# Kernel optimization log

Measured on AMD Instinct MI355X. Metric: run time of the kernel, lower is better.

Reference implementation:

```python
import jax, jax.numpy as jnp
import numpy as np

DIM = 192
NUM_HEADS = 8
EPS = 1e-12  # F.normalize default eps


def setup_inputs() -> dict:
    key = jax.random.key(0)
    ks = jax.random.split(key, 6)
    b, c, h, w = 8, DIM, 128, 128
    scale = 1.0 / np.sqrt(DIM)  # conv2d default init scale (approx)
    return {
        "input": jax.random.normal(ks[0], (b, c, h, w), dtype=jnp.float32),
        "color": jax.random.normal(ks[1], (b, c, h, w), dtype=jnp.float32),
        "Wq": jax.random.normal(ks[2], (DIM, DIM), dtype=jnp.float32) * scale,
        "Wk": jax.random.normal(ks[3], (DIM, DIM), dtype=jnp.float32) * scale,
        "Wv": jax.random.normal(ks[4], (DIM, DIM), dtype=jnp.float32) * scale,
        "Wo": jax.random.normal(ks[5], (DIM, DIM), dtype=jnp.float32) * scale,
    }


def _proj(x, W):
    # 1x1 conv (bias=False) == channel GEMM: [b,c,h,w] x [out,c] -> [b,out,h,w]
    return jnp.einsum('bchw,oc->bohw', x, W)


def _l2norm(x):
    n = jnp.sqrt(jnp.sum(x * x, axis=-1, keepdims=True))
    return x / jnp.maximum(n, EPS)


def reference(input, color, Wq, Wk, Wv, Wo):
    b, c, h, w = input.shape
    head = NUM_HEADS
    dh = c // head
    hw = h * w
    # q from color, k/v from input
    q = _proj(color, Wq).reshape(b, head, dh, hw)
    k = _proj(input, Wk).reshape(b, head, dh, hw)
    v = _proj(input, Wv).reshape(b, head, dh, hw)
    q = _l2norm(q)
    k = _l2norm(k)
    # transposed (channel) attention: [b,head,dh,dh]
    attn = jnp.einsum('bhcn,bhdn->bhcd', q, k)
    attn = jax.nn.softmax(attn, axis=-1)
    out = jnp.einsum('bhcd,bhdn->bhcn', attn, v)  # [b,head,dh,hw]
    out = out.reshape(b, c, h, w)
    return _proj(out, Wo)
```

## Files before the change

kernel.cpp:

```cpp
#include <hip/hip_runtime.h>
#include <hip/hip_bf16.h>


typedef __attribute__((ext_vector_type(4))) float f32x4;
typedef __attribute__((ext_vector_type(8))) short short8;

#define MFMA16(a, b, c) __builtin_amdgcn_mfma_f32_16x16x32_bf16((a), (b), (c), 0, 0, 0)

__device__ __forceinline__ unsigned int pack_rne(float a, float b) {
  unsigned int ua = __float_as_uint(a), ub = __float_as_uint(b);
  ua += 0x7fffu + ((ua >> 16) & 1u);
  ub += 0x7fffu + ((ub >> 16) & 1u);
  return (ua >> 16) | (ub & 0xffff0000u);
}
__device__ __forceinline__ unsigned short bf16u_rne(float x) {
  unsigned int u = __float_as_uint(x);
  u += 0x7fffu + ((u >> 16) & 1u);
  return (unsigned short)(u >> 16);
}
union S8U { short8 s; unsigned int u[4]; };
__device__ __forceinline__ short8 load_cvt8(const float* p) {
  f32x4 x = *(const f32x4*)p;
  f32x4 y = *(const f32x4*)(p + 4);
  S8U r;
  r.u[0] = pack_rne(x[0], x[1]);
  r.u[1] = pack_rne(x[2], x[3]);
  r.u[2] = pack_rne(y[0], y[1]);
  r.u[3] = pack_rne(y[2], y[3]);
  return r.s;
}

#define HW 16384
#define CDIM 192
#define NB 8
#define GSZ (CDIM * CDIM)
#define NTILE 300
#define NPART 32
#define NPH 8
#define BROW 144

__global__ void k0_wvt(const float* __restrict__ Wv, unsigned short* __restrict__ WvT) {
  int idx = blockIdx.x * 256 + threadIdx.x;
  if (idx < CDIM * CDIM) {
    int j = idx / CDIM, cp = idx % CDIM;
    WvT[idx] = bf16u_rne(Wv[(size_t)cp * CDIM + j]);
  }
}

__device__ __forceinline__ short8 bfrag(const char* buf, int row, int lg, int ks2) {
  return *(const short8*)(buf + row * BROW + ks2 * 64 + lg * 16);
}

template <int W>
__device__ __forceinline__ void pair_step(const char* bb, f32x4 (&acc)[25],
                                          int l15, int lg) {
#pragma unroll
  for (int ks2 = 0; ks2 < 2; ++ks2) {
    const short8 aT = bfrag(bb, W * 16 + l15, lg, ks2);
    const short8 aB = bfrag(bb, (23 - W) * 16 + l15, lg, ks2);
#pragma unroll
    for (int ct = W; ct < 24; ++ct) {
      const short8 b = bfrag(bb, ct * 16 + l15, lg, ks2);
      acc[ct - W] = MFMA16(aT, b, acc[ct - W]);
      if (ct >= 23 - W) acc[ct + 1] = MFMA16(aB, b, acc[ct + 1]);
    }
  }
}

__device__ __forceinline__ void pair_dispatch(int wp, const char* bb,
                                              f32x4 (&acc)[25], int l15, int lg) {
  switch (wp) {
    case 0: pair_step<0>(bb, acc, l15, lg); break;
    case 1: pair_step<1>(bb, acc, l15, lg); break;
    case 2: pair_step<2>(bb, acc, l15, lg); break;
    case 3: pair_step<3>(bb, acc, l15, lg); break;
    case 4: pair_step<4>(bb, acc, l15, lg); break;
    case 5: pair_step<5>(bb, acc, l15, lg); break;
    case 6: pair_step<6>(bb, acc, l15, lg); break;
    case 7: pair_step<7>(bb, acc, l15, lg); break;
    case 8: pair_step<8>(bb, acc, l15, lg); break;
    case 9: pair_step<9>(bb, acc, l15, lg); break;
    case 10: pair_step<10>(bb, acc, l15, lg); break;
    default: pair_step<11>(bb, acc, l15, lg); break;
  }
}

__global__ __launch_bounds__(768) void gram2_k(const float* __restrict__ input,
                                               const float* __restrict__ color,
                                               unsigned long long* __restrict__ part) {
  __shared__ __align__(16) char bbuf[384 * BROW];
  const int tid = threadIdx.x, wave = tid >> 6, lane = tid & 63;
  const int l15 = lane & 15, lg = (lane >> 4) & 3;
  const int strip = blockIdx.x, b = blockIdx.y;
  const int zrow = tid >> 1, half = tid & 1;
  const float* src = ((zrow < 192) ? (input + (size_t)zrow * HW)
                                   : (color + (size_t)(zrow - 192) * HW)) +
                     (size_t)b * CDIM * HW;
  const int col00 = strip * NPH * 64 + half * 32;

  f32x4 acc[25];
#pragma unroll
  for (int i = 0; i < 25; ++i) acc[i] = (f32x4){0.f, 0.f, 0.f, 0.f};

  f32x4 v0, v1, v2, v3, v4, v5, v6, v7;
  {
    const float* p = src + col00;
    v0 = *(const f32x4*)(p);
    v1 = *(const f32x4*)(p + 4);
    v2 = *(const f32x4*)(p + 8);
    v3 = *(const f32x4*)(p + 12);
    v4 = *(const f32x4*)(p + 16);
    v5 = *(const f32x4*)(p + 20);
    v6 = *(const f32x4*)(p + 24);
    v7 = *(const f32x4*)(p + 28);
  }

#pragma unroll 1
  for (int ph = 0; ph < NPH; ++ph) {
    __syncthreads();
    {
      char* dst = bbuf + zrow * BROW + half * 64;
      S8U pk;
      pk.u[0] = pack_rne(v0[0], v0[1]);
      pk.u[1] = pack_rne(v0[2], v0[3]);
      pk.u[2] = pack_rne(v1[0], v1[1]);
      pk.u[3] = pack_rne(v1[2], v1[3]);
      *(short8*)(dst) = pk.s;
      pk.u[0] = pack_rne(v2[0], v2[1]);
      pk.u[1] = pack_rne(v2[2], v2[3]);
      pk.u[2] = pack_rne(v3[0], v3[1]);
      pk.u[3] = pack_rne(v3[2], v3[3]);
      *(short8*)(dst + 16) = pk.s;
      pk.u[0] = pack_rne(v4[0], v4[1]);
      pk.u[1] = pack_rne(v4[2], v4[3]);
      pk.u[2] = pack_rne(v5[0], v5[1]);
      pk.u[3] = pack_rne(v5[2], v5[3]);
      *(short8*)(dst + 32) = pk.s;
      pk.u[0] = pack_rne(v6[0], v6[1]);
      pk.u[1] = pack_rne(v6[2], v6[3]);
      pk.u[2] = pack_rne(v7[0], v7[1]);
      pk.u[3] = pack_rne(v7[2], v7[3]);
      *(short8*)(dst + 48) = pk.s;
    }
    __syncthreads();
    if (ph + 1 < NPH) {
      const float* p = src + col00 + (ph + 1) * 64;
      v0 = *(const f32x4*)(p);
      v1 = *(const f32x4*)(p + 4);
      v2 = *(const f32x4*)(p + 8);
      v3 = *(const f32x4*)(p + 12);
      v4 = *(const f32x4*)(p + 16);
      v5 = *(const f32x4*)(p + 20);
      v6 = *(const f32x4*)(p + 24);
      v7 = *(const f32x4*)(p + 28);
    }
    pair_dispatch(wave, bbuf, acc, l15, lg);
  }

  unsigned long long* pbase = part + (size_t)(b * NPART + strip) * NTILE * 64;
#pragma unroll
  for (int s = 0; s < 25; ++s) {
    const unsigned long long pk =
        (unsigned long long)pack_rne(acc[s][0], acc[s][1]) |
        ((unsigned long long)pack_rne(acc[s][2], acc[s][3]) << 32);
    pbase[(size_t)(wave * 25 + s) * 64 + lane] = pk;
  }
}

template <int NP>
__global__ __launch_bounds__(256) void reduce_k(const unsigned long long* __restrict__ part,
                                                float* __restrict__ G) {
  const int b = blockIdx.y;
  const int T = blockIdx.x * 4 + (threadIdx.x >> 6);
  const int lane = threadIdx.x & 63;
  const unsigned long long* p = part + ((size_t)b * NP * NTILE + T) * 64 + lane;
  unsigned long long v[NP];
#pragma unroll
  for (int s = 0; s < NP; ++s) v[s] = p[(size_t)s * NTILE * 64];
  float s0 = 0.f, s1 = 0.f, s2 = 0.f, s3 = 0.f;
#pragma unroll
  for (int s = 0; s < NP; ++s) {
    const unsigned int lo = (unsigned int)v[s], hi = (unsigned int)(v[s] >> 32);
    s0 += __uint_as_float(lo << 16);
    s1 += __uint_as_float(lo & 0xffff0000u);
    s2 += __uint_as_float(hi << 16);
    s3 += __uint_as_float(hi & 0xffff0000u);
  }
  const int w = T / 25, s = T % 25;
  int rt, ct;
  if (s <= 23 - w) { rt = w; ct = w + s; }
  else { rt = 23 - w; ct = s - 1; }
  int type, gm, gn;
  if (ct < 12) { type = 2; gm = rt; gn = ct; }
  else if (rt < 12) { type = 0; gm = rt; gn = ct - 12; }
  else { type = 1; gm = rt - 12; gn = ct - 12; }
  float* Gm = G + ((size_t)type * NB + b) * GSZ;
  const int l15 = lane & 15, lg = lane >> 4;
  const int row0 = gm * 16 + lg * 4, col = gn * 16 + l15;
  const float sums[4] = {s0, s1, s2, s3};
#pragma unroll
  for (int r = 0; r < 4; ++r) Gm[(size_t)(row0 + r) * CDIM + col] = sums[r];
  if (type != 0 && rt != ct) {
#pragma unroll
    for (int r = 0; r < 4; ++r) Gm[(size_t)col * CDIM + (row0 + r)] = sums[r];
  }
}

__global__ __launch_bounds__(256) void k2a(const float* __restrict__ G,
                                           const float* __restrict__ Wq,
                                           const float* __restrict__ Wk,
                                           float* __restrict__ A_pre,
                                           float* __restrict__ nqk) {
  const int b = blockIdx.x, type = blockIdx.y;
  __shared__ __align__(16) unsigned short Hs[192][200];
  const int tid = threadIdx.x, wave = tid >> 6, lane = tid & 63;
  const int l15 = lane & 15, lg = lane >> 4, row0 = wave * 48;
  const float* W1 = (type == 2) ? Wk : Wq;
  const float* Gm = G + ((size_t)type * NB + b) * GSZ;

  f32x4 acc[3][12];
#pragma unroll
  for (int t = 0; t < 3; t++)
#pragma unroll
    for (int j = 0; j < 12; j++) acc[t][j] = (f32x4){0.f, 0.f, 0.f, 0.f};

  for (int ks = 0; ks < 192; ks += 32) {
    short8 afr[3];
#pragma unroll
    for (int t = 0; t < 3; t++)
      afr[t] = load_cvt8(W1 + (size_t)(row0 + t * 16 + l15) * CDIM + ks + lg * 8);
#pragma unroll
    for (int tj = 0; tj < 12; tj++) {
      short8 bfr = load_cvt8(Gm + (size_t)(tj * 16 + l15) * CDIM + ks + lg * 8);
#pragma unroll
      for (int t = 0; t < 3; t++) acc[t][tj] = MFMA16(afr[t], bfr, acc[t][tj]);
    }
  }
#pragma unroll
  for (int t = 0; t < 3; t++)
#pragma unroll
    for (int tj = 0; tj < 12; tj++)
#pragma unroll
      for (int r = 0; r < 4; r++)
        Hs[row0 + t * 16 + lg * 4 + r][tj * 16 + l15] = bf16u_rne(acc[t][tj][r]);
  __syncthreads();

  if (type == 0) {
    f32x4 a2[3][12];
#pragma unroll
    for (int t = 0; t < 3; t++)
#pragma unroll
      for (int j = 0; j < 12; j++) a2[t][j] = (f32x4){0.f, 0.f, 0.f, 0.f};
    for (int ks = 0; ks < 192; ks += 32) {
      short8 afr[3];
#pragma unroll
      for (int t = 0; t < 3; t++)
        afr[t] = *(const short8*)&Hs[row0 + t * 16 + l15][ks + lg * 8];
#pragma unroll
      for (int tj = 0; tj < 12; tj++) {
        short8 bfr = load_cvt8(Wk + (size_t)(tj * 16 + l15) * CDIM + ks + lg * 8);
#pragma unroll
        for (int t = 0; t < 3; t++) a2[t][tj] = MFMA16(afr[t], bfr, a2[t][tj]);
      }
    }
    float* Ab = A_pre + (size_t)b * GSZ;
#pragma unroll
    for (int t = 0; t < 3; t++)
#pragma unroll
      for (int tj = 0; tj < 12; tj++)
#pragma unroll
        for (int r = 0; r < 4; r++)
          Ab[(size_t)(row0 + t * 16 + lg * 4 + r) * CDIM + tj * 16 + l15] = a2[t][tj][r];
  } else {
    f32x4 a2[3];
#pragma unroll
    for (int t = 0; t < 3; t++) a2[t] = (f32x4){0.f, 0.f, 0.f, 0.f};
    for (int ks = 0; ks < 192; ks += 32) {
#pragma unroll
      for (int t = 0; t < 3; t++) {
        short8 afr = *(const short8*)&Hs[row0 + t * 16 + l15][ks + lg * 8];
        short8 bfr = load_cvt8(W1 + (size_t)(row0 + t * 16 + l15) * CDIM + ks + lg * 8);
        a2[t] = MFMA16(afr, bfr, a2[t]);
      }
    }
    float* dst = nqk + ((size_t)(type - 1) * NB + b) * CDIM;
#pragma unroll
    for (int t = 0; t < 3; t++)
#pragma unroll
      for (int r = 0; r < 4; r++)
        if (lg * 4 + r == l15) dst[row0 + t * 16 + l15] = a2[t][r];
  }
}

__global__ void k2b(const float* __restrict__ A_pre, const float* __restrict__ nqk,
                    float* __restrict__ attnw) {
  const int b = blockIdx.x, tid = threadIdx.x;
  const int h = tid >> 5, r = tid & 31;
  if (r >= 24) return;
  const float* Ab = A_pre + (size_t)b * GSZ;
  const float* nq = nqk + (size_t)b * CDIM;
  const float* nk = nqk + (size_t)(NB + b) * CDIM;
  const int c = h * 24 + r;
  const float qn = rsqrtf(fmaxf(nq[c], 1e-24f));
  float e[24];
  float mx = -1e30f;
#pragma unroll
  for (int d = 0; d < 24; d++) {
    float kn = rsqrtf(fmaxf(nk[h * 24 + d], 1e-24f));
    float l = Ab[(size_t)c * CDIM + h * 24 + d] * qn * kn;
    e[d] = l;
    mx = fmaxf(mx, l);
  }
  float s = 0.f;
#pragma unroll
  for (int d = 0; d < 24; d++) {
    float x = __expf(e[d] - mx);
    e[d] = x;
    s += x;
  }
  const float inv = 1.0f / s;
  float* dst = attnw + (((size_t)b * NB + h) * 24 + r) * 24;
#pragma unroll
  for (int d = 0; d < 24; d++) dst[d] = e[d] * inv;
}

__global__ __launch_bounds__(256) void k3(const float* __restrict__ attnw,
                                          const float* __restrict__ Wo,
                                          const unsigned short* __restrict__ WvT,
                                          unsigned short* __restrict__ Pbf) {
  const int b = blockIdx.x;
  __shared__ __align__(16) unsigned short AT[192][200];
  __shared__ __align__(16) unsigned short Ms[192][200];
  const int tid = threadIdx.x, wave = tid >> 6, lane = tid & 63;
  const int l15 = lane & 15, lg = lane >> 4, row0 = wave * 48;

  unsigned int* ATu = (unsigned int*)&AT[0][0];
  for (int i = tid; i < 192 * 100; i += 256) ATu[i] = 0u;
  __syncthreads();
  const float* at = attnw + (size_t)b * NB * 24 * 24;
  for (int i = tid; i < 4608; i += 256) {
    int h = i / 576, rem = i % 576, c = rem / 24, d = rem % 24;
    AT[h * 24 + d][h * 24 + c] = bf16u_rne(at[(h * 24 + c) * 24 + d]);
  }
  __syncthreads();

  f32x4 acc[3][12];
#pragma unroll
  for (int t = 0; t < 3; t++)
#pragma unroll
    for (int j = 0; j < 12; j++) acc[t][j] = (f32x4){0.f, 0.f, 0.f, 0.f};
  for (int ks = 0; ks < 192; ks += 32) {
    short8 afr[3];
#pragma unroll
    for (int t = 0; t < 3; t++)
      afr[t] = load_cvt8(Wo + (size_t)(row0 + t * 16 + l15) * CDIM + ks + lg * 8);
#pragma unroll
    for (int tj = 0; tj < 12; tj++) {
      short8 bfr = *(const short8*)&AT[tj * 16 + l15][ks + lg * 8];
#pragma unroll
      for (int t = 0; t < 3; t++) acc[t][tj] = MFMA16(afr[t], bfr, acc[t][tj]);
    }
  }
#pragma unroll
  for (int t = 0; t < 3; t++)
#pragma unroll
    for (int tj = 0; tj < 12; tj++)
#pragma unroll
      for (int r = 0; r < 4; r++)
        Ms[row0 + t * 16 + lg * 4 + r][tj * 16 + l15] = bf16u_rne(acc[t][tj][r]);
  __syncthreads();

  f32x4 a2[3][12];
#pragma unroll
  for (int t = 0; t < 3; t++)
#pragma unroll
    for (int j = 0; j < 12; j++) a2[t][j] = (f32x4){0.f, 0.f, 0.f, 0.f};
  for (int ks = 0; ks < 192; ks += 32) {
    short8 afr[3];
#pragma unroll
    for (int t = 0; t < 3; t++)
      afr[t] = *(const short8*)&Ms[row0 + t * 16 + l15][ks + lg * 8];
#pragma unroll
    for (int tj = 0; tj < 12; tj++) {
      short8 bfr = *(const short8*)(WvT + (size_t)(tj * 16 + l15) * CDIM + ks + lg * 8);
#pragma unroll
      for (int t = 0; t < 3; t++) a2[t][tj] = MFMA16(afr[t], bfr, a2[t][tj]);
    }
  }
  unsigned short* Pb = Pbf + (size_t)b * GSZ;
#pragma unroll
  for (int t = 0; t < 3; t++)
#pragma unroll
    for (int tj = 0; tj < 12; tj++)
#pragma unroll
      for (int r = 0; r < 4; r++)
        Pb[(size_t)(row0 + t * 16 + lg * 4 + r) * CDIM + tj * 16 + l15] = bf16u_rne(a2[t][tj][r]);
}

__global__ __launch_bounds__(256) void kD(const unsigned short* __restrict__ Pbf,
                                          const float* __restrict__ input,
                                          float* __restrict__ out) {
  const int nchunk = blockIdx.x, b = blockIdx.y;
  const int n0 = nchunk * 128;
  __shared__ __align__(16) char BsT[128 * 384];
  const int tid = threadIdx.x, wave = tid >> 6, lane = tid & 63;
  const int l15 = lane & 15, lg = lane >> 4, row0 = wave * 48;

  {
    const int n4 = (tid & 31) * 4;
    const int kb0 = (tid >> 5) * 4;
    const float* src = input + (size_t)b * CDIM * HW + n0 + n4;
    f32x4 w[24];
#pragma unroll
    for (int rnd = 0; rnd < 6; ++rnd)
#pragma unroll
      for (int j = 0; j < 4; ++j)
        w[rnd * 4 + j] = *(const f32x4*)(src + (size_t)(kb0 + rnd * 32 + j) * HW);
    __builtin_amdgcn_sched_barrier(0);
    char* bsb = BsT;
#pragma unroll
    for (int rnd = 0; rnd < 6; ++rnd) {
      const int kb = kb0 + rnd * 32;
#pragma unroll
      for (int i = 0; i < 4; ++i) {
        const int n = n4 + i;
        unsigned long long pk =
            (unsigned long long)pack_rne(w[rnd * 4 + 0][i], w[rnd * 4 + 1][i]) |
            ((unsigned long long)pack_rne(w[rnd * 4 + 2][i], w[rnd * 4 + 3][i]) << 32);
        *(unsigned long long*)(bsb + n * 384 + ((kb * 2) ^ ((n & 7) << 4))) = pk;
      }
    }
  }
  __syncthreads();

  f32x4 acc[3][8];
#pragma unroll
  for (int t = 0; t < 3; t++)
#pragma unroll
    for (int j = 0; j < 8; j++) acc[t][j] = (f32x4){0.f, 0.f, 0.f, 0.f};

  const unsigned short* Pb = Pbf + (size_t)b * GSZ;
#pragma unroll 2
  for (int ks = 0; ks < 6; ks++) {
    short8 afr[3];
#pragma unroll
    for (int t = 0; t < 3; t++)
      afr[t] = *(const short8*)(Pb + (size_t)(row0 + t * 16 + l15) * CDIM + ks * 32 + lg * 8);
#pragma unroll
    for (int tn = 0; tn < 8; tn++) {
      const int n = tn * 16 + l15;
      short8 bfr = *(const short8*)(BsT + n * 384 + ((ks * 64 + lg * 16) ^ ((n & 7) << 4)));
#pragma unroll
      for (int t = 0; t < 3; t++) acc[t][tn] = MFMA16(afr[t], bfr, acc[t][tn]);
    }
  }
  float* ob = out + (size_t)b * CDIM * HW + n0;
#pragma unroll
  for (int t = 0; t < 3; t++)
#pragma unroll
    for (int tn = 0; tn < 8; tn++)
#pragma unroll
      for (int r = 0; r < 4; r++) {
        const int m = row0 + t * 16 + lg * 4 + r;
        ob[(size_t)m * HW + tn * 16 + l15] = acc[t][tn][r];
      }
}

extern "C" void kernel_launch(void* const* d_in, const int* in_sizes, int n_in,
                              void* d_out, int out_size, void* d_ws, size_t ws_size,
                              hipStream_t stream) {
  const float* input = (const float*)d_in[0];
  const float* color = (const float*)d_in[1];
  const float* Wq = (const float*)d_in[2];
  const float* Wk = (const float*)d_in[3];
  const float* Wv = (const float*)d_in[4];
  const float* Wo = (const float*)d_in[5];
  float* out = (float*)d_out;
  char* ws = (char*)d_ws;

  const size_t OFF_G = 0;
  const size_t OFF_APRE = 3538944;
  const size_t OFF_NQK = OFF_APRE + 1179648;
  const size_t OFF_ATT = OFF_NQK + 12288;
  const size_t OFF_WVT = OFF_ATT + 147456;
  const size_t OFF_PBF = OFF_WVT + 73728;

  float* G = (float*)(ws + OFF_G);
  float* A_pre = (float*)(ws + OFF_APRE);
  float* nqk = (float*)(ws + OFF_NQK);
  float* attnw = (float*)(ws + OFF_ATT);
  unsigned short* WvT = (unsigned short*)(ws + OFF_WVT);
  unsigned short* Pbf = (unsigned short*)(ws + OFF_PBF);

  unsigned long long* part = (unsigned long long*)d_out;

  k0_wvt<<<dim3(144), dim3(256), 0, stream>>>(Wv, WvT);
  gram2_k<<<dim3(NPART, NB), dim3(768), 0, stream>>>(input, color, part);
  reduce_k<NPART><<<dim3(75, NB), dim3(256), 0, stream>>>(part, G);
  k2a<<<dim3(NB, 3), dim3(256), 0, stream>>>(G, Wq, Wk, A_pre, nqk);
  k2b<<<dim3(NB), dim3(256), 0, stream>>>(A_pre, nqk, attnw);
  k3<<<dim3(NB), dim3(256), 0, stream>>>(attnw, Wo, WvT, Pbf);
  kD<<<dim3(HW / 128, NB), dim3(256), 0, stream>>>(Pbf, input, out);
}
```

Baseline: 186.0 us.

## Restage gram kernel into 32-column chunks with four-thread-per-row loads

The Gram-matrix kernel now stages 32 spatial columns per phase (16 phases) instead of 64 columns (8 phases). Each thread loads 8 floats from both input and color for one row, rather than 32 floats from a single row. This shrinks the LDS row stride to 80 bytes and halves the register prefetch buffer, which may help occupancy or bank conflicts. In exchange it doubles the number of barrier-separated phases and issues smaller global reads per row segment.

Measured after the change: 180.9 us. -2.7%, faster.

```diff
diff --git a/kernel.cpp b/kernel.cpp
--- a/kernel.cpp
+++ b/kernel.cpp
@@ -36,8 +36,8 @@
 #define GSZ (CDIM * CDIM)
 #define NTILE 300
 #define NPART 32
-#define NPH 8
-#define BROW 144
+#define NCP 16
+#define BROW 80
 
 __global__ void k0_wvt(const float* __restrict__ Wv, unsigned short* __restrict__ WvT) {
   int idx = blockIdx.x * 256 + threadIdx.x;
@@ -47,23 +47,20 @@
   }
 }
 
-__device__ __forceinline__ short8 bfrag(const char* buf, int row, int lg, int ks2) {
-  return *(const short8*)(buf + row * BROW + ks2 * 64 + lg * 16);
+__device__ __forceinline__ short8 bfrag(const char* buf, int row, int lg) {
+  return *(const short8*)(buf + row * BROW + lg * 16);
 }
 
 template <int W>
 __device__ __forceinline__ void pair_step(const char* bb, f32x4 (&acc)[25],
                                           int l15, int lg) {
-#pragma unroll
-  for (int ks2 = 0; ks2 < 2; ++ks2) {
-    const short8 aT = bfrag(bb, W * 16 + l15, lg, ks2);
-    const short8 aB = bfrag(bb, (23 - W) * 16 + l15, lg, ks2);
-#pragma unroll
-    for (int ct = W; ct < 24; ++ct) {
-      const short8 b = bfrag(bb, ct * 16 + l15, lg, ks2);
-      acc[ct - W] = MFMA16(aT, b, acc[ct - W]);
-      if (ct >= 23 - W) acc[ct + 1] = MFMA16(aB, b, acc[ct + 1]);
-    }
+  const short8 aT = bfrag(bb, W * 16 + l15, lg);
+  const short8 aB = bfrag(bb, (23 - W) * 16 + l15, lg);
+#pragma unroll
+  for (int ct = W; ct < 24; ++ct) {
+    const short8 b = bfrag(bb, ct * 16 + l15, lg);
+    acc[ct - W] = MFMA16(aT, b, acc[ct - W]);
+    if (ct >= 23 - W) acc[ct + 1] = MFMA16(aB, b, acc[ct + 1]);
   }
 }
 
@@ -92,67 +89,47 @@
   const int tid = threadIdx.x, wave = tid >> 6, lane = tid & 63;
   const int l15 = lane & 15, lg = (lane >> 4) & 3;
   const int strip = blockIdx.x, b = blockIdx.y;
-  const int zrow = tid >> 1, half = tid & 1;
-  const float* src = ((zrow < 192) ? (input + (size_t)zrow * HW)
-                                   : (color + (size_t)(zrow - 192) * HW)) +
-                     (size_t)b * CDIM * HW;
-  const int col00 = strip * NPH * 64 + half * 32;
+  const int row = tid >> 2, sub = tid & 3;
+  const float* ip = input + (size_t)b * CDIM * HW + (size_t)row * HW;
+  const float* cp_ = color + (size_t)b * CDIM * HW + (size_t)row * HW;
+  const int ch0 = strip * NCP * 2;
 
   f32x4 acc[25];
 #pragma unroll
   for (int i = 0; i < 25; ++i) acc[i] = (f32x4){0.f, 0.f, 0.f, 0.f};
 
-  f32x4 v0, v1, v2, v3, v4, v5, v6, v7;
+  f32x4 vi0, vi1, vc0, vc1;
   {
-    const float* p = src + col00;
-    v0 = *(const f32x4*)(p);
-    v1 = *(const f32x4*)(p + 4);
-    v2 = *(const f32x4*)(p + 8);
-    v3 = *(const f32x4*)(p + 12);
-    v4 = *(const f32x4*)(p + 16);
-    v5 = *(const f32x4*)(p + 20);
-    v6 = *(const f32x4*)(p + 24);
-    v7 = *(const f32x4*)(p + 28);
+    const int colf = (ch0 + (sub >> 1)) * 16 + (sub & 1) * 8;
+    vi0 = *(const f32x4*)(ip + colf);
+    vi1 = *(const f32x4*)(ip + colf + 4);
+    vc0 = *(const f32x4*)(cp_ + colf);
+    vc1 = *(const f32x4*)(cp_ + colf + 4);
   }
 
 #pragma unroll 1
-  for (int ph = 0; ph < NPH; ++ph) {
+  for (int cpi = 0; cpi < NCP; ++cpi) {
     __syncthreads();
     {
-      char* dst = bbuf + zrow * BROW + half * 64;
       S8U pk;
-      pk.u[0] = pack_rne(v0[0], v0[1]);
-      pk.u[1] = pack_rne(v0[2], v0[3]);
-      pk.u[2] = pack_rne(v1[0], v1[1]);
-      pk.u[3] = pack_rne(v1[2], v1[3]);
-      *(short8*)(dst) = pk.s;
-      pk.u[0] = pack_rne(v2[0], v2[1]);
-      pk.u[1] = pack_rne(v2[2], v2[3]);
-      pk.u[2] = pack_rne(v3[0], v3[1]);
-      pk.u[3] = pack_rne(v3[2], v3[3]);
-      *(short8*)(dst + 16) = pk.s;
-      pk.u[0] = pack_rne(v4[0], v4[1]);
-      pk.u[1] = pack_rne(v4[2], v4[3]);
-      pk.u[2] = pack_rne(v5[0], v5[1]);
-      pk.u[3] = pack_rne(v5[2], v5[3]);
-      *(short8*)(dst + 32) = pk.s;
-      pk.u[0] = pack_rne(v6[0], v6[1]);
-      pk.u[1] = pack_rne(v6[2], v6[3]);
-      pk.u[2] = pack_rne(v7[0], v7[1]);
-      pk.u[3] = pack_rne(v7[2], v7[3]);
-      *(short8*)(dst + 48) = pk.s;
+      pk.u[0] = pack_rne(vi0[0], vi0[1]);
+      pk.u[1] = pack_rne(vi0[2], vi0[3]);
+      pk.u[2] = pack_rne(vi1[0], vi1[1]);
+      pk.u[3] = pack_rne(vi1[2], vi1[3]);
+      *(short8*)(bbuf + row * BROW + sub * 16) = pk.s;
+      pk.u[0] = pack_rne(vc0[0], vc0[1]);
+      pk.u[1] = pack_rne(vc0[2], vc0[3]);
+      pk.u[2] = pack_rne(vc1[0], vc1[1]);
+      pk.u[3] = pack_rne(vc1[2], vc1[3]);
+      *(short8*)(bbuf + (192 + row) * BROW + sub * 16) = pk.s;
     }
     __syncthreads();
-    if (ph + 1 < NPH) {
-      const float* p = src + col00 + (ph + 1) * 64;
-      v0 = *(const f32x4*)(p);
-      v1 = *(const f32x4*)(p + 4);
-      v2 = *(const f32x4*)(p + 8);
-      v3 = *(const f32x4*)(p + 12);
-      v4 = *(const f32x4*)(p + 16);
-      v5 = *(const f32x4*)(p + 20);
-      v6 = *(const f32x4*)(p + 24);
-      v7 = *(const f32x4*)(p + 28);
+    if (cpi + 1 < NCP) {
+      const int colf = (ch0 + 2 * (cpi + 1) + (sub >> 1)) * 16 + (sub & 1) * 8;
+      vi0 = *(const f32x4*)(ip + colf);
+      vi1 = *(const f32x4*)(ip + colf + 4);
+      vc0 = *(const f32x4*)(cp_ + colf);
+      vc1 = *(const f32x4*)(cp_ + colf + 4);
     }
     pair_dispatch(wave, bbuf, acc, l15, lg);
   }
```
